# Kernel optimization log

Hardware: AMD Instinct MI355X
Metric: run time of the kernel (lower is better)

Reference implementation:

```python
import jax, jax.numpy as jnp
import numpy as np

B, C, N, S, DCONV = 16, 128, 2000, 8, 4
DI = 2 * N            # mamba expand=2
DT_RANK = (N + 15) // 16


def setup_inputs() -> dict:
    key = jax.random.key(0)
    ks = jax.random.split(key, 10)
    r = lambda k, sh, s=0.02: jax.random.normal(k, sh, jnp.float32) * s
    return {
        "x": jax.random.normal(ks[0], (B, C, N, 1), jnp.float32),
        "bn1_g": jnp.ones((C,), jnp.float32), "bn1_b": jnp.zeros((C,), jnp.float32),
        "conv1_w": r(ks[1], (C, C)), "conv1_b": jnp.zeros((C,), jnp.float32),
        "ln_w": jnp.ones((N,), jnp.float32), "ln_b": jnp.zeros((N,), jnp.float32),
        "W_in": r(ks[2], (2 * DI, N)),
        "convm_w": r(ks[3], (DI, DCONV), 0.1), "convm_b": jnp.zeros((DI,), jnp.float32),
        "W_x": r(ks[4], (DT_RANK + 2 * S, DI)),
        "W_dt": r(ks[5], (DI, DT_RANK), 0.1), "b_dt": jnp.full((DI,), -2.0, jnp.float32),
        "A_log": jnp.log(jnp.broadcast_to(jnp.arange(1, S + 1, dtype=jnp.float32), (DI, S))),
        "D_p": jnp.ones((DI,), jnp.float32),
        "W_out": r(ks[6], (N, DI)),
        "bn3_g": jnp.ones((C,), jnp.float32), "bn3_b": jnp.zeros((C,), jnp.float32),
        "conv3_w": r(ks[7], (C, C)), "conv3_b": jnp.zeros((C,), jnp.float32),
    }


def _inorm(x, eps=1e-3):
    # InstanceNorm2d (no affine): per-sample, per-channel over spatial dims
    m = x.mean(axis=(2, 3), keepdims=True)
    v = x.var(axis=(2, 3), keepdims=True)
    return (x - m) * jax.lax.rsqrt(v + eps)


def _bnorm(x, g, b, eps=1e-5):
    # BatchNorm2d (training-mode stats) over (B, H, W) per channel
    m = x.mean(axis=(0, 2, 3), keepdims=True)
    v = x.var(axis=(0, 2, 3), keepdims=True)
    return (x - m) * jax.lax.rsqrt(v + eps) * g[None, :, None, None] + b[None, :, None, None]


def _block(x, g, b, w, cb):
    # InstanceNorm -> BatchNorm -> ReLU -> 1x1 Conv2d
    h = jax.nn.relu(_bnorm(_inorm(x), g, b))
    return jnp.einsum('bcnw,oc->bonw', h, w) + cb[None, :, None, None]


def _mamba(u, W_in, cw, cb, W_x, W_dt, b_dt, A_log, D_p, W_out):
    # u: [B, L, D] with L=C (seq), D=N (d_model)
    L = u.shape[1]
    xz = jnp.einsum('bld,ed->ble', u, W_in)          # [B,L,2*DI]
    xi, z = jnp.split(xz, 2, axis=-1)
    # depthwise causal conv1d along L (d_conv=4)
    xp = jnp.pad(xi, ((0, 0), (DCONV - 1, 0), (0, 0)))
    xc = sum(xp[:, k:k + L, :] * cw[:, k] for k in range(DCONV)) + cb
    xc = jax.nn.silu(xc)                             # [B,L,DI]
    xdbl = jnp.einsum('bld,ed->ble', xc, W_x)        # [B,L,dt_rank+2S]
    dt = jax.nn.softplus(jnp.einsum('blr,dr->bld', xdbl[..., :DT_RANK], W_dt) + b_dt)
    Bm = xdbl[..., DT_RANK:DT_RANK + S]              # [B,L,S]
    Cm = xdbl[..., DT_RANK + S:]                     # [B,L,S]
    A = -jnp.exp(A_log)                              # [DI,S]

    def step(h, inp):
        dt_l, B_l, C_l, u_l = inp                    # [B,DI],[B,S],[B,S],[B,DI]
        dA = jnp.exp(dt_l[..., None] * A)            # [B,DI,S]
        h = dA * h + (dt_l * u_l)[..., None] * B_l[:, None, :]
        return h, jnp.einsum('bds,bs->bd', h, C_l)

    seq = (jnp.swapaxes(dt, 0, 1), jnp.swapaxes(Bm, 0, 1),
           jnp.swapaxes(Cm, 0, 1), jnp.swapaxes(xc, 0, 1))
    h0 = jnp.zeros((u.shape[0], DI, S), u.dtype)
    _, ys = jax.lax.scan(step, h0, seq)              # ys: [L,B,DI]
    y = jnp.swapaxes(ys, 0, 1) + xc * D_p
    y = y * jax.nn.silu(z)
    return jnp.einsum('ble,de->bld', y, W_out)       # [B,L,D]


def reference(x, bn1_g, bn1_b, conv1_w, conv1_b, ln_w, ln_b, W_in, convm_w,
              convm_b, W_x, W_dt, b_dt, A_log, D_p, W_out, bn3_g, bn3_b,
              conv3_w, conv3_b):
    out = _block(x, bn1_g, bn1_b, conv1_w, conv1_b)[..., 0]   # [B,C,N]
    mu = out.mean(-1, keepdims=True)
    var = out.var(-1, keepdims=True)
    out_n = (out - mu) * jax.lax.rsqrt(var + 1e-5) * ln_w + ln_b  # LayerNorm(points)
    out = out + _mamba(out_n, W_in, convm_w, convm_b, W_x, W_dt, b_dt, A_log, D_p, W_out)
    out = _block(out[..., None], bn3_g, bn3_b, conv3_w, conv3_b)  # [B,C,N,1]
    return out + x
```

## Files before the change

### kernel.cpp

```cpp
#include <hip/hip_runtime.h>
#include <cmath>
#include <cstdint>

#define Bc   16
#define Cc   128
#define Nc   2000
#define Lc   128
#define DIc  4000
#define Sc   8
#define RKc  125
#define E2c  8000
#define EXc  141

#define KP1  2048
#define NP8  8192
#define KT8  32

__device__ __forceinline__ unsigned short f2bf(float f) {
  union { float f; unsigned int u; } v; v.f = f;
  unsigned int r = v.u + 0x7FFFu + ((v.u >> 16) & 1u);
  return (unsigned short)(r >> 16);
}

__global__ void inorm_stats(const float* __restrict__ in,
                            float* __restrict__ mout,
                            float* __restrict__ vout) {
  int bc = blockIdx.x;
  const float* p = in + (long)bc * Nc;
  float s = 0.f, sq = 0.f;
  for (int i = threadIdx.x; i < Nc; i += blockDim.x) {
    float x = p[i]; s += x; sq += x * x;
  }
  #pragma unroll
  for (int o = 32; o > 0; o >>= 1) {
    s  += __shfl_down(s, o, 64);
    sq += __shfl_down(sq, o, 64);
  }
  __shared__ float ss[4], sqq[4];
  int w = threadIdx.x >> 6, lane = threadIdx.x & 63;
  if (lane == 0) { ss[w] = s; sqq[w] = sq; }
  __syncthreads();
  if (threadIdx.x == 0) {
    s  = ss[0] + ss[1] + ss[2] + ss[3];
    sq = sqq[0] + sqq[1] + sqq[2] + sqq[3];
    float mean = s / Nc;
    float var  = sq / Nc - mean * mean;
    mout[bc] = mean; vout[bc] = var;
  }
}

__global__ void bn_scale(const float* __restrict__ v, float* __restrict__ bnsc) {
  int c = threadIdx.x;
  if (c >= Cc) return;
  float s = 0.f;
  for (int b = 0; b < Bc; b++) {
    float vv = v[b * Cc + c];
    s += vv / (vv + 1e-3f);
  }
  bnsc[c] = rsqrtf(s / Bc + 1e-5f);
}

__global__ void compute_h_t(const float* __restrict__ in,
                            const float* __restrict__ m,
                            const float* __restrict__ v,
                            const float* __restrict__ bnsc,
                            const float* __restrict__ g,
                            const float* __restrict__ bb,
                            unsigned short* __restrict__ hT) {
  int b  = blockIdx.y;
  int n0 = blockIdx.x * 64;
  __shared__ unsigned short tile[64][132];
  int t  = threadIdx.x;
  int nl = t & 63, cb = t >> 6;
  int n  = n0 + nl;
  #pragma unroll 4
  for (int p = 0; p < 32; p++) {
    int c = p * 4 + cb;
    float val = 0.f;
    if (n < Nc) {
      int bc = b * Cc + c;
      float xn = (in[(long)bc * Nc + n] - m[bc]) * rsqrtf(v[bc] + 1e-3f);
      val = fmaxf(xn * bnsc[c] * g[c] + bb[c], 0.f);
    }
    tile[nl][c] = f2bf(val);
  }
  __syncthreads();
  int r = t >> 2, c0 = (t & 3) * 32;
  int nr = n0 + r;
  if (nr < Nc) {
    unsigned int* dst = (unsigned int*)(hT + ((long)b * 2048 + nr) * 128 + c0);
    const unsigned short* src = &tile[r][c0];
    #pragma unroll
    for (int j = 0; j < 16; j++)
      dst[j] = *(const unsigned int*)(src + 2 * j);
  }
}

__global__ void reduce_slices(const float* __restrict__ sl, float* __restrict__ dst,
                              long stride, int ns, int total, int accum) {
  int i = blockIdx.x * 256 + threadIdx.x;
  if (i >= total) return;
  float s = accum ? dst[i] : 0.f;
  for (int k = 0; k < ns; k++) s += sl[(long)k * stride + i];
  dst[i] = s;
}

__global__ void reduce_xdbl(const float* __restrict__ sl,
                            float* __restrict__ xd,
                            unsigned short* __restrict__ xdb) {
  int i = blockIdx.x * 256 + threadIdx.x;
  if (i >= 2048 * 144) return;
  int row = i / 144, c = i - row * 144;
  float s = 0.f;
  if (c < EXc) {
    #pragma unroll
    for (int k = 0; k < 4; k++) s += sl[(long)k * (2048 * 256) + (long)row * 256 + c];
    xd[(long)row * EXc + c] = s;
  }
  if (c < 128) xdb[(long)row * 128 + c] = f2bf(c < RKc ? s : 0.f);
}

__global__ void cvt_pad_bf16(const float* __restrict__ src, unsigned short* __restrict__ dst,
                             int R, int Cdst, int Rsrc, int Csrc) {
  long i = (long)blockIdx.x * 256 + threadIdx.x;
  long total = (long)R * Cdst;
  if (i >= total) return;
  int r = (int)(i / Cdst), c = (int)(i - (long)r * Cdst);
  float v = (r < Rsrc && c < Csrc) ? src[(long)r * Csrc + c] : 0.f;
  dst[i] = f2bf(v);
}

__global__ void ln_rows(const float* __restrict__ in,
                        const float* __restrict__ lw,
                        const float* __restrict__ lb,
                        unsigned short* __restrict__ An) {
  int row = blockIdx.x;
  const float* p = in + (long)row * Nc;
  float s = 0.f, sq = 0.f;
  for (int i = threadIdx.x; i < Nc; i += blockDim.x) {
    float x = p[i]; s += x; sq += x * x;
  }
  #pragma unroll
  for (int o = 32; o > 0; o >>= 1) {
    s  += __shfl_down(s, o, 64);
    sq += __shfl_down(sq, o, 64);
  }
  __shared__ float ss[4], sqq[4];
  __shared__ float smean, srstd;
  int w = threadIdx.x >> 6, lane = threadIdx.x & 63;
  if (lane == 0) { ss[w] = s; sqq[w] = sq; }
  __syncthreads();
  if (threadIdx.x == 0) {
    s  = ss[0] + ss[1] + ss[2] + ss[3];
    sq = sqq[0] + sqq[1] + sqq[2] + sqq[3];
    float mean = s / Nc;
    float var  = sq / Nc - mean * mean;
    smean = mean; srstd = rsqrtf(var + 1e-5f);
  }
  __syncthreads();
  float mu = smean, rs = srstd;
  for (int i = threadIdx.x; i < KP1; i += blockDim.x) {
    float v = 0.f;
    if (i < Nc) v = (p[i] - mu) * rs * lw[i] + lb[i];
    An[(long)row * KP1 + i] = f2bf(v);
  }
}

typedef short v8s __attribute__((ext_vector_type(8)));
typedef float v4f __attribute__((ext_vector_type(4)));

typedef const __attribute__((address_space(1))) unsigned int* as1_cu32p;
typedef __attribute__((address_space(3))) unsigned int* as3_u32p;

__device__ __forceinline__ void gload_lds16(const unsigned short* g, unsigned short* l) {
  __builtin_amdgcn_global_load_lds((as1_cu32p)(uintptr_t)g,
                                   (as3_u32p)(uintptr_t)l, 16, 0, 0);
}

__global__ __launch_bounds__(256, 4)
void gemm_mfma_bt(const unsigned short* __restrict__ A,
                  const unsigned short* __restrict__ B,
                  float* C, int NN, int K, int lda, int ldb, int ldc,
                  long sA, long sB, long sC,
                  int KS, int Klen, long sliceStride,
                  int epi, const float* __restrict__ ebias,
                  const float* __restrict__ addp) {
  __shared__ unsigned short As[128 * 32];
  __shared__ unsigned short Bs[128 * 32];

  int z = blockIdx.z;
  int batch = z / KS, ks = z - batch * KS;
  const unsigned short* Ab = A + (long)batch * sA;
  const unsigned short* Bb = B + (long)batch * sB;
  float* Cs = C + (long)batch * sC + (long)ks * sliceStride;
  const float* X = addp ? addp + (long)batch * sC : nullptr;

  int k0 = ks * Klen;
  int kend = min(K, k0 + Klen);

  int i0 = blockIdx.y * 128;
  int j0 = blockIdx.x * 128;

  int t = threadIdx.x;
  int wave = t >> 6, lane = t & 63;
  int wm = wave >> 1, wn = wave & 1;

  int srow = lane >> 2;
  int scol = lane & 3;
  const unsigned short* gA0 = Ab + (long)(i0 + wave * 32 + srow) * lda + scol * 8;
  const unsigned short* gA1 = gA0 + (long)16 * lda;
  const unsigned short* gB0 = Bb + (long)(j0 + wave * 32 + srow) * ldb + scol * 8;
  const unsigned short* gB1 = gB0 + (long)16 * ldb;
  unsigned short* lA0 = As + (wave * 32) * 32;
  unsigned short* lA1 = As + (wave * 32 + 16) * 32;
  unsigned short* lB0 = Bs + (wave * 32) * 32;
  unsigned short* lB1 = Bs + (wave * 32 + 16) * 32;

  int fr = lane & 15;
  int kq = lane >> 4;

  v4f acc[4][4] = {};

  for (int kt = k0; kt < kend; kt += 32) {
    gload_lds16(gA0 + kt, lA0);
    gload_lds16(gA1 + kt, lA1);
    gload_lds16(gB0 + kt, lB0);
    gload_lds16(gB1 + kt, lB1);
    __syncthreads();

    v8s af[4], bfr[4];
    #pragma unroll
    for (int mt = 0; mt < 4; mt++)
      af[mt] = *(const v8s*)&As[(wm * 64 + mt * 16 + fr) * 32 + kq * 8];
    #pragma unroll
    for (int nt = 0; nt < 4; nt++)
      bfr[nt] = *(const v8s*)&Bs[(wn * 64 + nt * 16 + fr) * 32 + kq * 8];

    #pragma unroll
    for (int mt = 0; mt < 4; mt++)
      #pragma unroll
      for (int nt = 0; nt < 4; nt++)
        acc[mt][nt] = __builtin_amdgcn_mfma_f32_16x16x32_bf16(
            af[mt], bfr[nt], acc[mt][nt], 0, 0, 0);
    __syncthreads();
  }

  int orow = (lane >> 4) * 4;
  int ocol = lane & 15;
  #pragma unroll
  for (int mt = 0; mt < 4; mt++) {
    #pragma unroll
    for (int nt = 0; nt < 4; nt++) {
      int gi = i0 + wm * 64 + mt * 16 + orow;
      int gj = j0 + wn * 64 + nt * 16 + ocol;
      if (gj >= NN) continue;
      #pragma unroll
      for (int r = 0; r < 4; r++) {
        long idx = (long)(gi + r) * ldc + gj;
        float v = acc[mt][nt][r];
        if (epi == 1) {
          float tr = v + ebias[gj];
          v = fmaxf(tr, 0.f) + log1pf(__expf(-fabsf(tr)));
        } else if (epi == 2) {
          if (gj >= DIc) v = v / (1.f + __expf(-v));
        } else if (epi == 3) {
          v += ebias[gi + r];
          if (X) v += X[idx];
        }
        Cs[idx] = v;
      }
    }
  }
}

__global__ __launch_bounds__(512, 2)
void gemm_win_8ph(const unsigned short* __restrict__ A,
                  const unsigned short* __restrict__ B,
                  float* __restrict__ C) {
  __shared__ unsigned short As8[2 * 2 * 128 * 64];
  __shared__ unsigned short Bs8[2 * 2 * 128 * 64];

  const int lda = KP1, ldb = KP1, ldc = E2c;

  int i0 = blockIdx.y * 256;
  int j0 = blockIdx.x * 256;

  int t = threadIdx.x;
  int w = t >> 6, l = t & 63;
  int wm = w >> 2;
  int wn = w & 3;
  int w8 = w << 3;

  int rw     = w8 + (l >> 3);
  int scol16 = (l & 7) ^ ((l >> 3) & 7);
  const unsigned short* pA = A + (long)(i0 + rw) * lda + scol16 * 8;
  int gjrow = ((rw >> 5) << 6) + (rw & 31);
  const unsigned short* pB = B + (long)(j0 + gjrow) * ldb + scol16 * 8;

  int fr   = l & 15;
  int kq   = l >> 4;
  int inr0 = ((kq ^ (fr & 7)) << 4);
  int inr1 = inr0 ^ 64;

  const char* asb = (const char*)As8;
  const char* bsb = (const char*)Bs8;

  v4f acc[8][4] = {};
  v8s aF[4][2], bF[2][2][2];

#define ST_A(bufi, h, tile) do {                                              \
    int kt_ = ((tile) < KT8 ? (tile) : (KT8 - 1)) * 64;                       \
    gload_lds16(pA + (long)((h) * 64) * lda + kt_,                            \
                As8 + (size_t)((((bufi) * 2 + (h)) * 128 + w8) * 64));        \
    gload_lds16(pA + (long)(128 + (h) * 64) * lda + kt_,                      \
                As8 + (size_t)((((bufi) * 2 + (h)) * 128 + 64 + w8) * 64));   \
  } while (0)
#define ST_B(bufi, h, tile) do {                                              \
    int kt_ = ((tile) < KT8 ? (tile) : (KT8 - 1)) * 64;                       \
    gload_lds16(pB + (long)((h) * 32) * ldb + kt_,                            \
                Bs8 + (size_t)((((bufi) * 2 + (h)) * 128 + w8) * 64));        \
    gload_lds16(pB + (long)(128 + (h) * 32) * ldb + kt_,                      \
                Bs8 + (size_t)((((bufi) * 2 + (h)) * 128 + 64 + w8) * 64));   \
  } while (0)
#define LD_A(bufi, mh) do {                                                   \
    const char* ab_ = asb + (size_t)(((((bufi) * 2 + (mh)) * 128) + wm * 64 + fr) * 128); \
    aF[0][0] = *(const v8s*)(ab_ +    0 + inr0); aF[0][1] = *(const v8s*)(ab_ +    0 + inr1); \
    aF[1][0] = *(const v8s*)(ab_ + 2048 + inr0); aF[1][1] = *(const v8s*)(ab_ + 2048 + inr1); \
    aF[2][0] = *(const v8s*)(ab_ + 4096 + inr0); aF[2][1] = *(const v8s*)(ab_ + 4096 + inr1); \
    aF[3][0] = *(const v8s*)(ab_ + 6144 + inr0); aF[3][1] = *(const v8s*)(ab_ + 6144 + inr1); \
  } while (0)
#define LD_B(bufi, nh) do {                                                   \
    const char* bb_ = bsb + (size_t)(((((bufi) * 2 + (nh)) * 128) + wn * 32 + fr) * 128); \
    bF[nh][0][0] = *(const v8s*)(bb_ +    0 + inr0); bF[nh][0][1] = *(const v8s*)(bb_ +    0 + inr1); \
    bF[nh][1][0] = *(const v8s*)(bb_ + 2048 + inr0); bF[nh][1][1] = *(const v8s*)(bb_ + 2048 + inr1); \
  } while (0)
#define MM(mh, nh) do {                                                       \
    _Pragma("unroll")                                                         \
    for (int mt_ = 0; mt_ < 4; mt_++) {                                       \
      _Pragma("unroll")                                                       \
      for (int nt_ = 0; nt_ < 2; nt_++) {                                     \
        acc[(mh) * 4 + mt_][(nh) * 2 + nt_] = __builtin_amdgcn_mfma_f32_16x16x32_bf16( \
            aF[mt_][0], bF[nh][nt_][0], acc[(mh) * 4 + mt_][(nh) * 2 + nt_], 0, 0, 0); \
        acc[(mh) * 4 + mt_][(nh) * 2 + nt_] = __builtin_amdgcn_mfma_f32_16x16x32_bf16( \
            aF[mt_][1], bF[nh][nt_][1], acc[(mh) * 4 + mt_][(nh) * 2 + nt_], 0, 0, 0); \
      } }                                                                     \
  } while (0)
#define FENCE()   __asm__ volatile("" ::: "memory")
#define BARRIER() do { FENCE(); __builtin_amdgcn_s_barrier(); FENCE(); } while (0)
#define WAIT_LGKM0() do { __asm__ volatile("s_waitcnt lgkmcnt(0)" ::: "memory"); \
                          __builtin_amdgcn_sched_barrier(0); } while (0)
#define WAIT_VM(n) __asm__ volatile("s_waitcnt vmcnt(" #n ")" ::: "memory")

  ST_A(0, 0, 0); ST_B(0, 0, 0); ST_B(0, 1, 0); ST_A(0, 1, 0);
  ST_A(1, 0, 1); ST_B(1, 1, 1); ST_A(1, 1, 1);
  WAIT_VM(6);
  BARRIER();

  #pragma unroll 1
  for (int it = 0; it < KT8 / 2; ++it) {
    int u = 2 * it;
    LD_A(0, 0); LD_B(0, 0); ST_B(1, 0, u + 1);
    BARRIER(); WAIT_LGKM0();
    __builtin_amdgcn_s_setprio(1); MM(0, 0); __builtin_amdgcn_s_setprio(0);
    BARRIER();
    LD_B(0, 1); ST_A(0, 0, u + 2);
    BARRIER(); WAIT_LGKM0();
    __builtin_amdgcn_s_setprio(1); MM(0, 1); __builtin_amdgcn_s_setprio(0);
    BARRIER();
    LD_A(0, 1); ST_B(0, 1, u + 2);
    BARRIER(); WAIT_LGKM0();
    __builtin_amdgcn_s_setprio(1); MM(1, 1); __builtin_amdgcn_s_setprio(0);
    BARRIER();
    ST_A(0, 1, u + 2);
    BARRIER();
    __builtin_amdgcn_s_setprio(1); MM(1, 0); __builtin_amdgcn_s_setprio(0);
    WAIT_VM(6);
    BARRIER();
    LD_A(1, 0); LD_B(1, 0); ST_B(0, 0, u + 2);
    BARRIER(); WAIT_LGKM0();
    __builtin_amdgcn_s_setprio(1); MM(0, 0); __builtin_amdgcn_s_setprio(0);
    BARRIER();
    LD_B(1, 1); ST_A(1, 0, u + 3);
    BARRIER(); WAIT_LGKM0();
    __builtin_amdgcn_s_setprio(1); MM(0, 1); __builtin_amdgcn_s_setprio(0);
    BARRIER();
    LD_A(1, 1); ST_B(1, 1, u + 3);
    BARRIER(); WAIT_LGKM0();
    __builtin_amdgcn_s_setprio(1); MM(1, 1); __builtin_amdgcn_s_setprio(0);
    BARRIER();
    ST_A(1, 1, u + 3);
    BARRIER();
    __builtin_amdgcn_s_setprio(1); MM(1, 0); __builtin_amdgcn_s_setprio(0);
    WAIT_VM(6);
    BARRIER();
  }
  WAIT_VM(0);

  int orow4 = (l >> 4) * 4;
  int ocol  = l & 15;
  #pragma unroll
  for (int m = 0; m < 8; m++) {
    int gi = i0 + wm * 128 + m * 16 + orow4;
    #pragma unroll
    for (int n = 0; n < 4; n++) {
      int gj = j0 + wn * 64 + n * 16 + ocol;
      if (gj >= E2c) continue;
      #pragma unroll
      for (int r = 0; r < 4; r++) {
        float v = acc[m][n][r];
        if (gj >= DIc) v = v / (1.f + __expf(-v));
        C[(long)(gi + r) * ldc + gj] = v;
      }
    }
  }
#undef ST_A
#undef ST_B
#undef LD_A
#undef LD_B
#undef MM
#undef FENCE
#undef BARRIER
#undef WAIT_LGKM0
#undef WAIT_VM
}

__global__ void dwconv_silu(const float* __restrict__ xz,
                            const float4* __restrict__ cw,
                            const float* __restrict__ cb,
                            float* __restrict__ xc,
                            unsigned short* __restrict__ xcb, int total) {
  int i = blockIdx.x * 256 + threadIdx.x;
  if (i >= total) return;
  int d  = i % DIc;
  int bl = i / DIc;
  int l  = bl % Lc;
  int b  = bl / Lc;
  float4 w = cw[d];
  float acc = cb[d];
  long rowbase = (long)(b * Lc) * E2c + d;
  int l0 = l - 3;
  if (l0     >= 0) acc += xz[rowbase + (long)l0       * E2c] * w.x;
  if (l0 + 1 >= 0) acc += xz[rowbase + (long)(l0 + 1) * E2c] * w.y;
  if (l0 + 2 >= 0) acc += xz[rowbase + (long)(l0 + 2) * E2c] * w.z;
  acc += xz[rowbase + (long)l * E2c] * w.w;
  float sv = acc / (1.f + __expf(-acc));
  xc[i] = sv;
  xcb[i] = f2bf(sv);
}

#define SCU 4
__global__ __launch_bounds__(256)
void scan_kernel(const float* __restrict__ dtv,
                 const float* __restrict__ xdbl,
                 const float* __restrict__ xc,
                 const float* __restrict__ xzf,
                 const float* __restrict__ A_log,
                 const float* __restrict__ D_p,
                 unsigned short* __restrict__ yb) {
  int d = blockIdx.x * 256 + threadIdx.x;
  int b = blockIdx.y;
  if (d >= DIc) return;
  float Av[Sc];
  #pragma unroll
  for (int s = 0; s < Sc; s++) Av[s] = -__expf(A_log[d * Sc + s]);
  float Dp = D_p[d];
  float h[Sc];
  #pragma unroll
  for (int s = 0; s < Sc; s++) h[s] = 0.f;

  long base  = (long)(b * Lc) * DIc + d;
  long zbase = (long)(b * Lc) * E2c + DIc + d;
  const float* xrow = xdbl + (long)(b * Lc) * EXc + RKc;

  float d0[SCU], u0[SCU], z0[SCU], B0[SCU][Sc], C0[SCU][Sc];
  float d1[SCU], u1[SCU], z1[SCU], B1[SCU][Sc], C1[SCU][Sc];

#define LOADG(g, dd, uu, zz, BB, CC)                                        \
  { int l0_ = (g) * SCU;                                                    \
    _Pragma("unroll")                                                       \
    for (int u = 0; u < SCU; u++) {                                         \
      long idx = base + (long)(l0_ + u) * DIc;                              \
      dd[u] = dtv[idx];                                                     \
      uu[u] = xc[idx];                                                      \
      zz[u] = xzf[zbase + (long)(l0_ + u) * E2c];                           \
      const float* xr = xrow + (long)(l0_ + u) * EXc;                       \
      _Pragma("unroll")                                                     \
      for (int s = 0; s < Sc; s++) { BB[u][s] = xr[s]; CC[u][s] = xr[Sc + s]; } \
    } }

#define COMPG(g, dd, uu, zz, BB, CC)                                        \
  { int l0_ = (g) * SCU;                                                    \
    _Pragma("unroll")                                                       \
    for (int u = 0; u < SCU; u++) {                                         \
      float dv = dd[u], uv = uu[u];                                         \
      float du = dv * uv;                                                   \
      float p = 0.f;                                                        \
      _Pragma("unroll")                                                     \
      for (int s = 0; s < Sc; s++) {                                        \
        float dA = __expf(dv * Av[s]);                                      \
        h[s] = dA * h[s] + du * BB[u][s];                                   \
        p += h[s] * CC[u][s];                                               \
      }                                                                     \
      yb[base + (long)(l0_ + u) * DIc] = f2bf((p + uv * Dp) * zz[u]);       \
    } }

  LOADG(0, d0, u0, z0, B0, C0);
  #pragma unroll 1
  for (int g = 0; g < Lc / SCU; g += 2) {
    LOADG(g + 1, d1, u1, z1, B1, C1);
    COMPG(g, d0, u0, z0, B0, C0);
    if (g + 2 < Lc / SCU) LOADG(g + 2, d0, u0, z0, B0, C0);
    COMPG(g + 1, d1, u1, z1, B1, C1);
  }
#undef LOADG
#undef COMPG
}

extern "C" void kernel_launch(void* const* d_in, const int* in_sizes, int n_in,
                              void* d_out, int out_size, void* d_ws, size_t ws_size,
                              hipStream_t stream) {
  const float* x       = (const float*)d_in[0];
  const float* bn1_g   = (const float*)d_in[1];
  const float* bn1_b   = (const float*)d_in[2];
  const float* conv1_w = (const float*)d_in[3];
  const float* conv1_b = (const float*)d_in[4];
  const float* ln_w    = (const float*)d_in[5];
  const float* ln_b    = (const float*)d_in[6];
  const float* W_in    = (const float*)d_in[7];
  const float* convm_w = (const float*)d_in[8];
  const float* convm_b = (const float*)d_in[9];
  const float* W_x     = (const float*)d_in[10];
  const float* W_dt    = (const float*)d_in[11];
  const float* b_dt    = (const float*)d_in[12];
  const float* A_log   = (const float*)d_in[13];
  const float* D_p     = (const float*)d_in[14];
  const float* W_out   = (const float*)d_in[15];
  const float* bn3_g   = (const float*)d_in[16];
  const float* bn3_b   = (const float*)d_in[17];
  const float* conv3_w = (const float*)d_in[18];
  const float* conv3_b = (const float*)d_in[19];
  float* out = (float*)d_out;
  float* ws  = (float*)d_ws;

  const int TOT  = Bc * Cc * Nc;
  const int ROWS = Bc * Lc;

  float* m1    = ws;
  float* v1    = ws + 2048;
  float* bnsc  = ws + 4096;
  float* h     = ws + 8192;
  float* out1  = h    + (long)TOT;
  float* outn  = out1 + (long)TOT;
  float* xz    = outn + (long)TOT;
  float* xc    = xz   + (long)ROWS * E2c;
  float* xdbl  = xc   + (long)ROWS * DIc;
  float* dtb   = xdbl + (long)ROWS * EXc;

  unsigned short* An      = (unsigned short*)outn;
  unsigned short* Bwin8   = (unsigned short*)xc;
  unsigned short* Bwx     = (unsigned short*)outn;
  unsigned short* Bwdt    = (unsigned short*)(outn + 512000);
  float*          xdbl_sl = outn + 800000;
  unsigned short* xdbl_b  = (unsigned short*)(outn + 2900000);
  unsigned short* W1b     = (unsigned short*)(outn + 3100000);
  unsigned short* W3b     = (unsigned short*)(outn + 3200000);
  unsigned short* hT      = (unsigned short*)h;
  unsigned short* xcb     = (unsigned short*)h;
  unsigned short* Bwout   = (unsigned short*)h;
  unsigned short* yb      = (unsigned short*)out;
  float*          wout_sl = xz;

  dim3 b256(256);
  int gElem = (TOT + 255) / 256;

  inorm_stats<<<dim3(Bc * Cc), b256, 0, stream>>>(x, m1, v1);
  bn_scale<<<dim3(1), dim3(128), 0, stream>>>(v1, bnsc);
  compute_h_t<<<dim3(32, Bc), b256, 0, stream>>>(x, m1, v1, bnsc, bn1_g, bn1_b, hT);
  cvt_pad_bf16<<<dim3(64), b256, 0, stream>>>(conv1_w, W1b, 128, 128, Cc, Cc);
  {
    dim3 g(16, 1, Bc);
    gemm_mfma_bt<<<g, b256, 0, stream>>>(W1b, hT, out1, Nc, 128, 128, 128, Nc,
                                         0L, 2048L * 128, (long)Cc * Nc,
                                         1, 128, 0L, 3, conv1_b, nullptr);
  }

  ln_rows<<<dim3(ROWS), b256, 0, stream>>>(out1, ln_w, ln_b, An);

  {
    long tot = (long)NP8 * KP1;
    cvt_pad_bf16<<<dim3((unsigned)((tot + 255) / 256)), b256, 0, stream>>>(
        W_in, Bwin8, NP8, KP1, E2c, Nc);
  }

  gemm_win_8ph<<<dim3(NP8 / 256, ROWS / 256), dim3(512), 0, stream>>>(An, Bwin8, xz);

  cvt_pad_bf16<<<dim3((256 * 4000 + 255) / 256), b256, 0, stream>>>(
      W_x, Bwx, 256, 4000, EXc, DIc);
  cvt_pad_bf16<<<dim3((4096 * 128 + 255) / 256), b256, 0, stream>>>(
      W_dt, Bwdt, 4096, 128, DIc, RKc);

  {
    int tot = ROWS * DIc;
    dwconv_silu<<<dim3((tot + 255) / 256), b256, 0, stream>>>(
        xz, (const float4*)convm_w, convm_b, xc, xcb, tot);
  }

  {
    dim3 g(2, ROWS / 128, 4);
    gemm_mfma_bt<<<g, b256, 0, stream>>>(xcb, Bwx, xdbl_sl, 256, DIc,
                                         DIc, DIc, 256, 0L, 0L, 0L,
                                         4, 1024, 2048L * 256, 0, nullptr, nullptr);
    int tot = 2048 * 144;
    reduce_xdbl<<<dim3((tot + 255) / 256), b256, 0, stream>>>(xdbl_sl, xdbl, xdbl_b);
  }

  {
    dim3 g(4096 / 128, ROWS / 128, 1);
    gemm_mfma_bt<<<g, b256, 0, stream>>>(xdbl_b, Bwdt, dtb, DIc, 128,
                                         128, 128, DIc, 0L, 0L, 0L,
                                         1, 128, 0L, 1, b_dt, nullptr);
  }

  {
    long tot = (long)2048 * DIc;
    cvt_pad_bf16<<<dim3((unsigned)((tot + 255) / 256)), b256, 0, stream>>>(
        W_out, Bwout, 2048, DIc, Nc, DIc);
  }

  scan_kernel<<<dim3((DIc + 255) / 256, Bc), b256, 0, stream>>>(
      dtb, xdbl, xc, xz, A_log, D_p, yb);

  {
    dim3 g(2048 / 128, ROWS / 128, 2);
    gemm_mfma_bt<<<g, b256, 0, stream>>>(yb, Bwout, wout_sl, Nc, DIc, DIc, DIc, Nc,
                                         0L, 0L, 0L, 2, 2048, (long)TOT,
                                         0, nullptr, nullptr);
    reduce_slices<<<dim3(gElem), b256, 0, stream>>>(
        wout_sl, out1, (long)TOT, 2, TOT, 1);
  }

  inorm_stats<<<dim3(Bc * Cc), b256, 0, stream>>>(out1, m1, v1);
  bn_scale<<<dim3(1), dim3(128), 0, stream>>>(v1, bnsc);
  compute_h_t<<<dim3(32, Bc), b256, 0, stream>>>(out1, m1, v1, bnsc, bn3_g, bn3_b, hT);
  cvt_pad_bf16<<<dim3(64), b256, 0, stream>>>(conv3_w, W3b, 128, 128, Cc, Cc);
  {
    dim3 g(16, 1, Bc);
    gemm_mfma_bt<<<g, b256, 0, stream>>>(W3b, hT, out, Nc, 128, 128, 128, Nc,
                                         0L, 2048L * 128, (long)Cc * Nc,
                                         1, 128, 0L, 3, conv3_b, x);
  }
}
```

Before: 633.2 us.

## Add pipelined 8-phase W_out GEMM with split-K and fuse small conversion kernels

Replaces the generic MFMA GEMM for the W_out projection with a dedicated 256x256-tile, 512-thread, double-buffered 8-phase kernel split four ways along K, padding the K tail by loading from a zero buffer. The four partial slices are then summed into the residual by reduce_slices. Separately, the BN-scale computation is folded into compute_h_t, and the weight bf16 conversions are merged into fewer launches (conv1/conv3 together, W_x with W_dt, W_out with the x_dbl reduction). The aim is higher GEMM throughput and lower launch overhead, at the cost of writing and reading more split-K slices and relying on the zero-padding buffer being valid.

```diff
diff --git a/kernel.cpp b/kernel.cpp
--- a/kernel.cpp
+++ b/kernel.cpp
@@ -49,28 +49,27 @@
   }
 }
 
-__global__ void bn_scale(const float* __restrict__ v, float* __restrict__ bnsc) {
-  int c = threadIdx.x;
-  if (c >= Cc) return;
-  float s = 0.f;
-  for (int b = 0; b < Bc; b++) {
-    float vv = v[b * Cc + c];
-    s += vv / (vv + 1e-3f);
-  }
-  bnsc[c] = rsqrtf(s / Bc + 1e-5f);
-}
-
 __global__ void compute_h_t(const float* __restrict__ in,
                             const float* __restrict__ m,
                             const float* __restrict__ v,
-                            const float* __restrict__ bnsc,
                             const float* __restrict__ g,
                             const float* __restrict__ bb,
                             unsigned short* __restrict__ hT) {
   int b  = blockIdx.y;
   int n0 = blockIdx.x * 64;
   __shared__ unsigned short tile[64][132];
+  __shared__ float bnsc_s[128];
   int t  = threadIdx.x;
+  if (t < 128) {
+    float s = 0.f;
+    #pragma unroll
+    for (int bb2 = 0; bb2 < Bc; bb2++) {
+      float vv = v[bb2 * Cc + t];
+      s += vv / (vv + 1e-3f);
+    }
+    bnsc_s[t] = rsqrtf(s / Bc + 1e-5f);
+  }
+  __syncthreads();
   int nl = t & 63, cb = t >> 6;
   int n  = n0 + nl;
   #pragma unroll 4
@@ -80,7 +79,7 @@
     if (n < Nc) {
       int bc = b * Cc + c;
       float xn = (in[(long)bc * Nc + n] - m[bc]) * rsqrtf(v[bc] + 1e-3f);
-      val = fmaxf(xn * bnsc[c] * g[c] + bb[c], 0.f);
+      val = fmaxf(xn * bnsc_s[c] * g[c] + bb[c], 0.f);
     }
     tile[nl][c] = f2bf(val);
   }
@@ -105,19 +104,28 @@
   dst[i] = s;
 }
 
-__global__ void reduce_xdbl(const float* __restrict__ sl,
-                            float* __restrict__ xd,
-                            unsigned short* __restrict__ xdb) {
+__global__ void reduce_xdbl_cvt_wout(const float* __restrict__ sl,
+                                     float* __restrict__ xd,
+                                     unsigned short* __restrict__ xdb,
+                                     const float* __restrict__ Wout,
+                                     unsigned short* __restrict__ bwout) {
   int i = blockIdx.x * 256 + threadIdx.x;
-  if (i >= 2048 * 144) return;
-  int row = i / 144, c = i - row * 144;
-  float s = 0.f;
-  if (c < EXc) {
-    #pragma unroll
-    for (int k = 0; k < 4; k++) s += sl[(long)k * (2048 * 256) + (long)row * 256 + c];
-    xd[(long)row * EXc + c] = s;
-  }
-  if (c < 128) xdb[(long)row * 128 + c] = f2bf(c < RKc ? s : 0.f);
+  if (i < 2048 * 144) {
+    int row = i / 144, c = i - row * 144;
+    float s = 0.f;
+    if (c < EXc) {
+      #pragma unroll
+      for (int k = 0; k < 4; k++) s += sl[(long)k * (2048 * 256) + (long)row * 256 + c];
+      xd[(long)row * EXc + c] = s;
+    }
+    if (c < 128) xdb[(long)row * 128 + c] = f2bf(c < RKc ? s : 0.f);
+  } else {
+    int j = i - 2048 * 144;
+    if (j < 2048 * 4000) {
+      int r = j / 4000, c = j - r * 4000;
+      bwout[j] = f2bf(r < Nc ? Wout[(long)r * 4000 + c] : 0.f);
+    }
+  }
 }
 
 __global__ void cvt_pad_bf16(const float* __restrict__ src, unsigned short* __restrict__ dst,
@@ -128,6 +136,28 @@
   int r = (int)(i / Cdst), c = (int)(i - (long)r * Cdst);
   float v = (r < Rsrc && c < Csrc) ? src[(long)r * Csrc + c] : 0.f;
   dst[i] = f2bf(v);
+}
+
+__global__ void cvt_convw2(const float* __restrict__ w1, const float* __restrict__ w3,
+                           unsigned short* __restrict__ d1, unsigned short* __restrict__ d3) {
+  int i = blockIdx.x * 256 + threadIdx.x;
+  if (i < 16384) d1[i] = f2bf(w1[i]);
+  else if (i < 32768) d3[i - 16384] = f2bf(w3[i - 16384]);
+}
+
+__global__ void cvt_wx_wdt(const float* __restrict__ Wx, const float* __restrict__ Wdt,
+                           unsigned short* __restrict__ bwx, unsigned short* __restrict__ bwdt) {
+  int i = blockIdx.x * 256 + threadIdx.x;
+  if (i < 256 * 4000) {
+    int r = i / 4000, c = i - r * 4000;
+    bwx[i] = f2bf(r < EXc ? Wx[(long)r * 4000 + c] : 0.f);
+  } else {
+    int j = i - 256 * 4000;
+    if (j < 4096 * 128) {
+      int r = j >> 7, c = j & 127;
+      bwdt[j] = f2bf((r < DIc && c < RKc) ? Wdt[(long)r * RKc + c] : 0.f);
+    }
+  }
 }
 
 __global__ void ln_rows(const float* __restrict__ in,
@@ -272,6 +302,23 @@
     }
   }
 }
+
+#define MM(mh, nh) do {                                                       \
+    _Pragma("unroll")                                                         \
+    for (int mt_ = 0; mt_ < 4; mt_++) {                                       \
+      _Pragma("unroll")                                                       \
+      for (int nt_ = 0; nt_ < 2; nt_++) {                                     \
+        acc[(mh) * 4 + mt_][(nh) * 2 + nt_] = __builtin_amdgcn_mfma_f32_16x16x32_bf16( \
+            aF[mt_][0], bF[nh][nt_][0], acc[(mh) * 4 + mt_][(nh) * 2 + nt_], 0, 0, 0); \
+        acc[(mh) * 4 + mt_][(nh) * 2 + nt_] = __builtin_amdgcn_mfma_f32_16x16x32_bf16( \
+            aF[mt_][1], bF[nh][nt_][1], acc[(mh) * 4 + mt_][(nh) * 2 + nt_], 0, 0, 0); \
+      } }                                                                     \
+  } while (0)
+#define FENCE()   __asm__ volatile("" ::: "memory")
+#define BARRIER() do { FENCE(); __builtin_amdgcn_s_barrier(); FENCE(); } while (0)
+#define WAIT_LGKM0() do { __asm__ volatile("s_waitcnt lgkmcnt(0)" ::: "memory"); \
+                          __builtin_amdgcn_sched_barrier(0); } while (0)
+#define WAIT_VM(n) __asm__ volatile("s_waitcnt vmcnt(" #n ")" ::: "memory")
 
 __global__ __launch_bounds__(512, 2)
 void gemm_win_8ph(const unsigned short* __restrict__ A,
@@ -334,22 +381,6 @@
     bF[nh][0][0] = *(const v8s*)(bb_ +    0 + inr0); bF[nh][0][1] = *(const v8s*)(bb_ +    0 + inr1); \
     bF[nh][1][0] = *(const v8s*)(bb_ + 2048 + inr0); bF[nh][1][1] = *(const v8s*)(bb_ + 2048 + inr1); \
   } while (0)
-#define MM(mh, nh) do {                                                       \
-    _Pragma("unroll")                                                         \
-    for (int mt_ = 0; mt_ < 4; mt_++) {                                       \
-      _Pragma("unroll")                                                       \
-      for (int nt_ = 0; nt_ < 2; nt_++) {                                     \
-        acc[(mh) * 4 + mt_][(nh) * 2 + nt_] = __builtin_amdgcn_mfma_f32_16x16x32_bf16( \
-            aF[mt_][0], bF[nh][nt_][0], acc[(mh) * 4 + mt_][(nh) * 2 + nt_], 0, 0, 0); \
-        acc[(mh) * 4 + mt_][(nh) * 2 + nt_] = __builtin_amdgcn_mfma_f32_16x16x32_bf16( \
-            aF[mt_][1], bF[nh][nt_][1], acc[(mh) * 4 + mt_][(nh) * 2 + nt_], 0, 0, 0); \
-      } }                                                                     \
-  } while (0)
-#define FENCE()   __asm__ volatile("" ::: "memory")
-#define BARRIER() do { FENCE(); __builtin_amdgcn_s_barrier(); FENCE(); } while (0)
-#define WAIT_LGKM0() do { __asm__ volatile("s_waitcnt lgkmcnt(0)" ::: "memory"); \
-                          __builtin_amdgcn_sched_barrier(0); } while (0)
-#define WAIT_VM(n) __asm__ volatile("s_waitcnt vmcnt(" #n ")" ::: "memory")
 
   ST_A(0, 0, 0); ST_B(0, 0, 0); ST_B(0, 1, 0); ST_A(0, 1, 0);
   ST_A(1, 0, 1); ST_B(1, 1, 1); ST_A(1, 1, 1);
@@ -417,12 +448,146 @@
 #undef ST_B
 #undef LD_A
 #undef LD_B
+}
+
+__global__ __launch_bounds__(512, 2)
+void gemm_wout_8ph(const unsigned short* __restrict__ A,
+                   const unsigned short* __restrict__ B,
+                   float* __restrict__ C,
+                   const unsigned short* __restrict__ zsrc) {
+  __shared__ unsigned short As8[2 * 2 * 128 * 64];
+  __shared__ unsigned short Bs8[2 * 2 * 128 * 64];
+
+  const int lda = 4000, ldb = 4000;
+
+  int i0 = blockIdx.y * 256;
+  int j0 = blockIdx.x * 256;
+  int ks = blockIdx.z;
+  int k0t = ks * 16;
+
+  int t = threadIdx.x;
+  int w = t >> 6, l = t & 63;
+  int wm = w >> 2;
+  int wn = w & 3;
+  int w8 = w << 3;
+
+  int rw     = w8 + (l >> 3);
+  int scol16 = (l & 7) ^ ((l >> 3) & 7);
+  const unsigned short* pA = A + (long)(i0 + rw) * lda + scol16 * 8;
+  int gjrow = ((rw >> 5) << 6) + (rw & 31);
+  const unsigned short* pB = B + (long)(j0 + gjrow) * ldb + scol16 * 8;
+
+  int fr   = l & 15;
+  int kq   = l >> 4;
+  int inr0 = ((kq ^ (fr & 7)) << 4);
+  int inr1 = inr0 ^ 64;
+
+  const char* asb = (const char*)As8;
+  const char* bsb = (const char*)Bs8;
+
+  v4f acc[8][4] = {};
+  v8s aF[4][2], bF[2][2][2];
+
+#define ST_A2(bufi, h, lt) do {                                               \
+    int gk_ = k0t + (((lt) < 16) ? (lt) : 15);                                \
+    bool pad_ = (gk_ >= 62) && (gk_ == 63 || scol16 >= 4);                    \
+    const unsigned short* s0_ = pad_ ? zsrc : pA + (long)((h) * 64) * lda + gk_ * 64;   \
+    const unsigned short* s1_ = pad_ ? zsrc : pA + (long)(128 + (h) * 64) * lda + gk_ * 64; \
+    gload_lds16(s0_, As8 + (size_t)((((bufi) * 2 + (h)) * 128 + w8) * 64));   \
+    gload_lds16(s1_, As8 + (size_t)((((bufi) * 2 + (h)) * 128 + 64 + w8) * 64)); \
+  } while (0)
+#define ST_B2(bufi, h, lt) do {                                               \
+    int gk_ = k0t + (((lt) < 16) ? (lt) : 15);                                \
+    bool pad_ = (gk_ >= 62) && (gk_ == 63 || scol16 >= 4);                    \
+    const unsigned short* s0_ = pad_ ? zsrc : pB + (long)((h) * 32) * ldb + gk_ * 64;   \
+    const unsigned short* s1_ = pad_ ? zsrc : pB + (long)(128 + (h) * 32) * ldb + gk_ * 64; \
+    gload_lds16(s0_, Bs8 + (size_t)((((bufi) * 2 + (h)) * 128 + w8) * 64));   \
+    gload_lds16(s1_, Bs8 + (size_t)((((bufi) * 2 + (h)) * 128 + 64 + w8) * 64)); \
+  } while (0)
+#define LD_A2(bufi, mh) do {                                                  \
+    const char* ab_ = asb + (size_t)(((((bufi) * 2 + (mh)) * 128) + wm * 64 + fr) * 128); \
+    aF[0][0] = *(const v8s*)(ab_ +    0 + inr0); aF[0][1] = *(const v8s*)(ab_ +    0 + inr1); \
+    aF[1][0] = *(const v8s*)(ab_ + 2048 + inr0); aF[1][1] = *(const v8s*)(ab_ + 2048 + inr1); \
+    aF[2][0] = *(const v8s*)(ab_ + 4096 + inr0); aF[2][1] = *(const v8s*)(ab_ + 4096 + inr1); \
+    aF[3][0] = *(const v8s*)(ab_ + 6144 + inr0); aF[3][1] = *(const v8s*)(ab_ + 6144 + inr1); \
+  } while (0)
+#define LD_B2(bufi, nh) do {                                                  \
+    const char* bb_ = bsb + (size_t)(((((bufi) * 2 + (nh)) * 128) + wn * 32 + fr) * 128); \
+    bF[nh][0][0] = *(const v8s*)(bb_ +    0 + inr0); bF[nh][0][1] = *(const v8s*)(bb_ +    0 + inr1); \
+    bF[nh][1][0] = *(const v8s*)(bb_ + 2048 + inr0); bF[nh][1][1] = *(const v8s*)(bb_ + 2048 + inr1); \
+  } while (0)
+
+  ST_A2(0, 0, 0); ST_B2(0, 0, 0); ST_B2(0, 1, 0); ST_A2(0, 1, 0);
+  ST_A2(1, 0, 1); ST_B2(1, 1, 1); ST_A2(1, 1, 1);
+  WAIT_VM(6);
+  BARRIER();
+
+  #pragma unroll 1
+  for (int it = 0; it < 8; ++it) {
+    int u = 2 * it;
+    LD_A2(0, 0); LD_B2(0, 0); ST_B2(1, 0, u + 1);
+    BARRIER(); WAIT_LGKM0();
+    __builtin_amdgcn_s_setprio(1); MM(0, 0); __builtin_amdgcn_s_setprio(0);
+    BARRIER();
+    LD_B2(0, 1); ST_A2(0, 0, u + 2);
+    BARRIER(); WAIT_LGKM0();
+    __builtin_amdgcn_s_setprio(1); MM(0, 1); __builtin_amdgcn_s_setprio(0);
+    BARRIER();
+    LD_A2(0, 1); ST_B2(0, 1, u + 2);
+    BARRIER(); WAIT_LGKM0();
+    __builtin_amdgcn_s_setprio(1); MM(1, 1); __builtin_amdgcn_s_setprio(0);
+    BARRIER();
+    ST_A2(0, 1, u + 2);
+    BARRIER();
+    __builtin_amdgcn_s_setprio(1); MM(1, 0); __builtin_amdgcn_s_setprio(0);
+    WAIT_VM(6);
+    BARRIER();
+    LD_A2(1, 0); LD_B2(1, 0); ST_B2(0, 0, u + 2);
+    BARRIER(); WAIT_LGKM0();
+    __builtin_amdgcn_s_setprio(1); MM(0, 0); __builtin_amdgcn_s_setprio(0);
+    BARRIER();
+    LD_B2(1, 1); ST_A2(1, 0, u + 3);
+    BARRIER(); WAIT_LGKM0();
+    __builtin_amdgcn_s_setprio(1); MM(0, 1); __builtin_amdgcn_s_setprio(0);
+    BARRIER();
+    LD_A2(1, 1); ST_B2(1, 1, u + 3);
+    BARRIER(); WAIT_LGKM0();
+    __builtin_amdgcn_s_setprio(1); MM(1, 1); __builtin_amdgcn_s_setprio(0);
+    BARRIER();
+    ST_A2(1, 1, u + 3);
+    BARRIER();
+    __builtin_amdgcn_s_setprio(1); MM(1, 0); __builtin_amdgcn_s_setprio(0);
+    WAIT_VM(6);
+    BARRIER();
+  }
+  WAIT_VM(0);
+
+  float* Cs = C + (long)ks * ((long)2048 * Nc);
+  int orow4 = (l >> 4) * 4;
+  int ocol  = l & 15;
+  #pragma unroll
+  for (int m = 0; m < 8; m++) {
+    int gi = i0 + wm * 128 + m * 16 + orow4;
+    #pragma unroll
+    for (int n = 0; n < 4; n++) {
+      int gj = j0 + wn * 64 + n * 16 + ocol;
+      if (gj >= Nc) continue;
+      #pragma unroll
+      for (int r = 0; r < 4; r++)
+        Cs[(long)(gi + r) * Nc + gj] = acc[m][n][r];
+    }
+  }
+#undef ST_A2
+#undef ST_B2
+#undef LD_A2
+#undef LD_B2
+}
+
 #undef MM
 #undef FENCE
 #undef BARRIER
 #undef WAIT_LGKM0
 #undef WAIT_VM
-}
 
 __global__ void dwconv_silu(const float* __restrict__ xz,
                             const float4* __restrict__ cw,
@@ -547,7 +712,6 @@
 
   float* m1    = ws;
   float* v1    = ws + 2048;
-  float* bnsc  = ws + 4096;
   float* h     = ws + 8192;
   float* out1  = h    + (long)TOT;
   float* outn  = out1 + (long)TOT;
@@ -569,14 +733,15 @@
   unsigned short* Bwout   = (unsigned short*)h;
   unsigned short* yb      = (unsigned short*)out;
   float*          wout_sl = xz;
+  const unsigned short* zsrc = (const unsigned short*)(outn + 768000);
 
   dim3 b256(256);
   int gElem = (TOT + 255) / 256;
 
+  cvt_convw2<<<dim3(128), b256, 0, stream>>>(conv1_w, conv3_w, W1b, W3b);
+
   inorm_stats<<<dim3(Bc * Cc), b256, 0, stream>>>(x, m1, v1);
-  bn_scale<<<dim3(1), dim3(128), 0, stream>>>(v1, bnsc);
-  compute_h_t<<<dim3(32, Bc), b256, 0, stream>>>(x, m1, v1, bnsc, bn1_g, bn1_b, hT);
-  cvt_pad_bf16<<<dim3(64), b256, 0, stream>>>(conv1_w, W1b, 128, 128, Cc, Cc);
+  compute_h_t<<<dim3(32, Bc), b256, 0, stream>>>(x, m1, v1, bn1_g, bn1_b, hT);
   {
     dim3 g(16, 1, Bc);
     gemm_mfma_bt<<<g, b256, 0, stream>>>(W1b, hT, out1, Nc, 128, 128, 128, Nc,
@@ -594,10 +759,8 @@
 
   gemm_win_8ph<<<dim3(NP8 / 256, ROWS / 256), dim3(512), 0, stream>>>(An, Bwin8, xz);
 
-  cvt_pad_bf16<<<dim3((256 * 4000 + 255) / 256), b256, 0, stream>>>(
-      W_x, Bwx, 256, 4000, EXc, DIc);
-  cvt_pad_bf16<<<dim3((4096 * 128 + 255) / 256), b256, 0, stream>>>(
-      W_dt, Bwdt, 4096, 128, DIc, RKc);
+  cvt_wx_wdt<<<dim3((256 * 4000 + 4096 * 128 + 255) / 256), b256, 0, stream>>>(
+      W_x, W_dt, Bwx, Bwdt);
 
   {
     int tot = ROWS * DIc;
@@ -610,8 +773,12 @@
     gemm_mfma_bt<<<g, b256, 0, stream>>>(xcb, Bwx, xdbl_sl, 256, DIc,
                                          DIc, DIc, 256, 0L, 0L, 0L,
                                          4, 1024, 2048L * 256, 0, nullptr, nullptr);
-    int tot = 2048 * 144;
-    reduce_xdbl<<<dim3((tot + 255) / 256), b256, 0, stream>>>(xdbl_sl, xdbl, xdbl_b);
+  }
+
+  {
+    int tot = 2048 * 144 + 2048 * 4000;
+    reduce_xdbl_cvt_wout<<<dim3((tot + 255) / 256), b256, 0, stream>>>(
+        xdbl_sl, xdbl, xdbl_b, W_out, Bwout);
   }
 
   {
@@ -621,28 +788,15 @@
                                          1, 128, 0L, 1, b_dt, nullptr);
   }
 
-  {
-    long tot = (long)2048 * DIc;
-    cvt_pad_bf16<<<dim3((unsigned)((tot + 255) / 256)), b256, 0, stream>>>(
-        W_out, Bwout, 2048, DIc, Nc, DIc);
-  }
-
   scan_kernel<<<dim3((DIc + 255) / 256, Bc), b256, 0, stream>>>(
       dtb, xdbl, xc, xz, A_log, D_p, yb);
 
-  {
-    dim3 g(2048 / 128, ROWS / 128, 2);
-    gemm_mfma_bt<<<g, b256, 0, stream>>>(yb, Bwout, wout_sl, Nc, DIc, DIc, DIc, Nc,
-                                         0L, 0L, 0L, 2, 2048, (long)TOT,
-                                         0, nullptr, nullptr);
-    reduce_slices<<<dim3(gElem), b256, 0, stream>>>(
-        wout_sl, out1, (long)TOT, 2, TOT, 1);
-  }
+  gemm_wout_8ph<<<dim3(8, 8, 4), dim3(512), 0, stream>>>(yb, Bwout, wout_sl, zsrc);
+  reduce_slices<<<dim3(gElem), b256, 0, stream>>>(
+      wout_sl, out1, (long)TOT, 4, TOT, 1);
 
   inorm_stats<<<dim3(Bc * Cc), b256, 0, stream>>>(out1, m1, v1);
-  bn_scale<<<dim3(1), dim3(128), 0, stream>>>(v1, bnsc);
-  compute_h_t<<<dim3(32, Bc), b256, 0, stream>>>(out1, m1, v1, bnsc, bn3_g, bn3_b, hT);
-  cvt_pad_bf16<<<dim3(64), b256, 0, stream>>>(conv3_w, W3b, 128, 128, Cc, Cc);
+  compute_h_t<<<dim3(32, Bc), b256, 0, stream>>>(out1, m1, v1, bn3_g, bn3_b, hT);
   {
     dim3 g(16, 1, Bc);
     gemm_mfma_bt<<<g, b256, 0, stream>>>(W3b, hT, out, Nc, 128, 128, 128, Nc,
```

Measured after the change: 715.7 us. +13.0%, slower.
